# Kernel tuning notes

Hardware: AMD Instinct MI355X
Metric: run time of the kernel (lower is better)

The kernel has to match this reference:

```python
import jax, jax.numpy as jnp
import numpy as np

B, M, L, IN_C, MID_C, OUT_C = 1, 128, 256, 256, 32, 128


def setup_inputs() -> dict:
    key = jax.random.key(0)
    k_x, k_proj, k_final = jax.random.split(key, 3)
    return {
        "x1d": jax.random.normal(k_x, (B, M, L, IN_C), dtype=jnp.float32),
        "norm_w": jnp.ones((IN_C,), dtype=jnp.float32),
        "norm_b": jnp.zeros((IN_C,), dtype=jnp.float32),
        "proj_w": jax.random.normal(k_proj, (2 * MID_C, IN_C), dtype=jnp.float32) * 0.02,
        "proj_b": jnp.zeros((2 * MID_C,), dtype=jnp.float32),
        "final_w": jax.random.normal(k_final, (OUT_C, MID_C * MID_C), dtype=jnp.float32) * 0.02,
        "final_b": jnp.zeros((OUT_C,), dtype=jnp.float32),
    }


def reference(x1d, norm_w, norm_b, proj_w, proj_b, final_w, final_b):
    # LayerNorm over channel dim
    mu = jnp.mean(x1d, axis=-1, keepdims=True)
    var = jnp.mean(jnp.square(x1d - mu), axis=-1, keepdims=True)
    x = (x1d - mu) * jax.lax.rsqrt(var + 1e-5) * norm_w + norm_b

    mid_c = proj_w.shape[0] // 2
    # Linear -> (b, m, L, 2*mid_c); view (..., mid_c, 2); chunk & squeeze:
    # i = interleaved even channels, j = interleaved odd channels
    p = jnp.einsum('bmlc,dc->bmld', x, proj_w) + proj_b
    p = p.reshape(*p.shape[:-1], mid_c, 2)
    i, j = p[..., 0], p[..., 1]          # each (b, m, L, mid_c)

    m = x1d.shape[1]
    # Outer product mean over the MSA (m) dimension -> (b, L, L, mid_c, mid_c)
    x2d = jnp.einsum('bmix,bmjy->bijxy', i, j) / m

    b, li, lj = x2d.shape[0], x2d.shape[1], x2d.shape[2]
    flat = x2d.reshape(b, li, lj, mid_c * mid_c)
    out = jnp.einsum('bijf,of->bijo', flat, final_w) + final_b
    return out
```

## Files before the change

### kernel.cpp

```cpp
#include <hip/hip_runtime.h>

#define DEVINL __device__ __forceinline__

typedef float  f32x4_t  __attribute__((ext_vector_type(4)));
typedef float  f32x16_t __attribute__((ext_vector_type(16)));
typedef short  bf16x8_t __attribute__((ext_vector_type(8)));

#define MFMA16(a,b,c) __builtin_amdgcn_mfma_f32_16x16x32_bf16((a),(b),(c),0,0,0)
#define MFMA32(a,b,c) __builtin_amdgcn_mfma_f32_32x32x16_bf16((a),(b),(c),0,0,0)

DEVINL unsigned short f2bf(float f) {
  union { float f; unsigned u; } v; v.f = f;
  unsigned r = v.u + 0x7fffu + ((v.u >> 16) & 1u);
  return (unsigned short)(r >> 16);
}


__global__ __launch_bounds__(256) void kA(const float* __restrict__ x,
                                          const float* __restrict__ nw,
                                          const float* __restrict__ nb,
                                          const float* __restrict__ pw,
                                          const float* __restrict__ pb,
                                          const float* __restrict__ fw,
                                          unsigned short* __restrict__ Wb,
                                          unsigned short* __restrict__ Ig,
                                          unsigned short* __restrict__ Jg) {
  if (blockIdx.x >= 1024) {
    int i = (blockIdx.x - 1024) * 256 + threadIdx.x;
    float4 v = ((const float4*)fw)[i];
    int o  = i >> 8;
    int f0 = (i & 255) * 4;
    ushort4 u;
    u.x = f2bf(v.x); u.y = f2bf(v.y); u.z = f2bf(v.z); u.w = f2bf(v.w);
    size_t off = (size_t)((o >> 5) * 64 + (f0 >> 4)) * 512 + (o & 31) * 16 + ((f0 >> 3) & 1) * 8 + (f0 & 7);
    *(ushort4*)&Wb[off] = u;
    return;
  }
  __shared__ unsigned short xnl[32 * 264];
  __shared__ unsigned short pwl[64 * 264];
  __shared__ unsigned short ep[64 * 36];
  const int tid  = threadIdx.x;
  const int wv   = tid >> 6;
  const int lane = tid & 63;
  const int q    = lane >> 4;
  const int ln16 = lane & 15;
  const int l    = blockIdx.x & 255;
  const int m0   = (blockIdx.x >> 8) * 32;

  const float4* xs = (const float4*)x;
  float4 v[8];
#pragma unroll
  for (int i = 0; i < 8; i++) {
    int row = m0 + i * 4 + wv;
    v[i] = xs[row * 16384 + l * 64 + lane];
  }
  float4 nw4 = ((const float4*)nw)[lane];
  float4 nb4 = ((const float4*)nb)[lane];

#pragma unroll
  for (int i = 0; i < 8; i++) {
    float s  = v[i].x + v[i].y + v[i].z + v[i].w;
    float ss = v[i].x * v[i].x + v[i].y * v[i].y + v[i].z * v[i].z + v[i].w * v[i].w;
#pragma unroll
    for (int off = 32; off > 0; off >>= 1) {
      s  += __shfl_xor(s, off);
      ss += __shfl_xor(ss, off);
    }
    float mu  = s * (1.0f / 256.0f);
    float var = ss * (1.0f / 256.0f) - mu * mu;
    float rs  = rsqrtf(var + 1e-5f);
    ushort4 u;
    u.x = f2bf((v[i].x - mu) * rs * nw4.x + nb4.x);
    u.y = f2bf((v[i].y - mu) * rs * nw4.y + nb4.y);
    u.z = f2bf((v[i].z - mu) * rs * nw4.z + nb4.z);
    u.w = f2bf((v[i].w - mu) * rs * nw4.w + nb4.w);
    *(ushort4*)&xnl[(i * 4 + wv) * 264 + lane * 4] = u;
  }

  const float4* ps = (const float4*)pw;
#pragma unroll
  for (int i = 0; i < 16; i++) {
    float4 w4 = ps[i * 256 + tid];
    ushort4 u;
    u.x = f2bf(w4.x); u.y = f2bf(w4.y); u.z = f2bf(w4.z); u.w = f2bf(w4.w);
    *(ushort4*)&pwl[(i * 4 + wv) * 264 + lane * 4] = u;
  }
  __syncthreads();

  const int rt = wv & 1;
  const int db = (wv >> 1) * 32;
  f32x4_t acc[2] = {{0.f, 0.f, 0.f, 0.f}, {0.f, 0.f, 0.f, 0.f}};
#pragma unroll
  for (int kc = 0; kc < 8; kc++) {
    bf16x8_t a  = *(const bf16x8_t*)&xnl[(rt * 16 + ln16) * 264 + kc * 32 + q * 8];
    bf16x8_t b0 = *(const bf16x8_t*)&pwl[(db + ln16) * 264 + kc * 32 + q * 8];
    bf16x8_t b1 = *(const bf16x8_t*)&pwl[(db + 16 + ln16) * 264 + kc * 32 + q * 8];
    acc[0] = MFMA16(a, b0, acc[0]);
    acc[1] = MFMA16(a, b1, acc[1]);
  }

#pragma unroll
  for (int t2 = 0; t2 < 2; t2++) {
    int d = db + t2 * 16 + ln16;
    float bias  = pb[d];
    float scale = (d & 1) ? 1.0f : (1.0f / 128.0f);
#pragma unroll
    for (int r = 0; r < 4; r++) {
      int mloc = rt * 16 + q * 4 + r;
      ep[d * 36 + mloc] = f2bf((acc[t2][r] + bias) * scale);
    }
  }
  __syncthreads();

  const int h  = tid >> 3;
  const int m4 = tid & 7;
  const size_t off = (size_t)(l * 8 + (m0 >> 4) + (m4 >> 2)) * 512 + h * 16 + ((m4 >> 1) & 1) * 8 + (m4 & 1) * 4;
  ushort4 vi = *(const ushort4*)&ep[(2 * h) * 36 + m4 * 4];
  *(ushort4*)&Ig[off] = vi;
  ushort4 vj = *(const ushort4*)&ep[(2 * h + 1) * 36 + m4 * 4];
  *(ushort4*)&Jg[off] = vj;
}

__global__ __launch_bounds__(512, 2) void kB(const unsigned short* __restrict__ Ig,
                                             const unsigned short* __restrict__ Jg,
                                             const unsigned short* __restrict__ Wb,
                                             const float* __restrict__ fb,
                                             float* __restrict__ out) {
  extern __shared__ unsigned short fl[];
  const int tid  = threadIdx.x;
  const int w    = tid >> 6;
  const int lane = tid & 63;
  const int ln32 = lane & 31;
  const int h    = lane >> 5;
  const int p    = blockIdx.x >> 3;
  const int t    = blockIdx.x & 7;

  bf16x8_t af[2][8];
#pragma unroll
  for (int il = 0; il < 2; il++)
#pragma unroll
    for (int mc = 0; mc < 8; mc++)
      af[il][mc] = *(const bf16x8_t*)&Ig[(size_t)((p * 2 + il) * 8 + mc) * 512 + ln32 * 16 + h * 8];

  const unsigned short* Jbase = Jg + (size_t)(t * 32 + w * 4) * 4096 + ln32 * 16 + h * 8;
  const int eo = ln32 & 7;
  const int oc = ln32 >> 3;

  bf16x8_t bf[2][8];
#pragma unroll
  for (int mc = 0; mc < 8; mc++) bf[0][mc] = *(const bf16x8_t*)&Jbase[mc * 512];

#pragma unroll
  for (int s = 0; s < 4; s++) {
    if (s < 3) {
#pragma unroll
      for (int mc = 0; mc < 8; mc++)
        bf[(s + 1) & 1][mc] = *(const bf16x8_t*)&Jbase[(s + 1) * 4096 + mc * 512];
    }
    f32x16_t a0, a1;
#pragma unroll
    for (int i = 0; i < 16; i++) { a0[i] = 0.f; a1[i] = 0.f; }
#pragma unroll
    for (int mc = 0; mc < 8; mc++) {
      a0 = MFMA32(af[0][mc], bf[s & 1][mc], a0);
      a1 = MFMA32(af[1][mc], bf[s & 1][mc], a1);
    }
    const int fr = w * 4 + s;
    unsigned short* fr0 = &fl[fr * 1032 + eo];
#pragma unroll
    for (int reg = 0; reg < 16; reg++) {
      int xx  = (reg & 3) + 8 * (reg >> 2) + 4 * h;
      int cp  = ((xx * 4 + oc) ^ (((xx >> 2) & 3) * 5)) * 8;
      fr0[cp]         = f2bf(a0[reg]);
      fr0[33024 + cp] = f2bf(a1[reg]);
    }
  }
  __syncthreads();

  const int il = w >> 2;
  const int ot = w & 3;
  const unsigned short* Wp  = Wb + (size_t)(ot * 64) * 512 + ln32 * 16 + h * 8;
  const unsigned short* flp = fl + il * 33024 + ln32 * 1032;

  f32x16_t oa;
#pragma unroll
  for (int i = 0; i < 16; i++) oa[i] = 0.f;

#define LDA(kc) (*(const bf16x8_t*)&flp[((((kc) >> 1) * 4 + ((kc) & 1) * 2 + h) ^ ((((kc) >> 3) & 3) * 5)) * 8])
  bf16x8_t a0 = LDA(0);
  bf16x8_t b0 = *(const bf16x8_t*)&Wp[0];
  bf16x8_t b1 = *(const bf16x8_t*)&Wp[512];
#pragma unroll 8
  for (int kc = 0; kc < 64; kc++) {
    bf16x8_t an = a0, bn = b1;
    if (kc < 63) an = LDA(kc + 1);
    if (kc < 62) bn = *(const bf16x8_t*)&Wp[(kc + 2) * 512];
    oa = MFMA32(a0, b0, oa);
    a0 = an; b0 = b1; b1 = bn;
  }
#undef LDA

  float bias = fb[ot * 32 + ln32];
  float* op = out + ((size_t)(p * 2 + il) * 256 + t * 32) * 128 + ot * 32 + ln32;
#pragma unroll
  for (int reg = 0; reg < 16; reg++) {
    int row = (reg & 3) + 8 * (reg >> 2) + 4 * h;
    op[row * 128] = oa[reg] + bias;
  }
}

extern "C" void kernel_launch(void* const* d_in, const int* in_sizes, int n_in,
                              void* d_out, int out_size, void* d_ws, size_t ws_size,
                              hipStream_t stream) {
  const float* x1d     = (const float*)d_in[0];
  const float* norm_w  = (const float*)d_in[1];
  const float* norm_b  = (const float*)d_in[2];
  const float* proj_w  = (const float*)d_in[3];
  const float* proj_b  = (const float*)d_in[4];
  const float* final_w = (const float*)d_in[5];
  const float* final_b = (const float*)d_in[6];
  float* outp          = (float*)d_out;

  unsigned short* Wb  = (unsigned short*)d_ws;
  unsigned short* Igp = Wb + 131072;
  unsigned short* Jgp = Igp + 1048576;

  const int kb_lds = 2 * 32 * 1032 * 2;
  hipFuncSetAttribute((const void*)kB, hipFuncAttributeMaxDynamicSharedMemorySize, kb_lds);

  kA<<<1152, 256, 0, stream>>>(x1d, norm_w, norm_b, proj_w, proj_b, final_w, Wb, Igp, Jgp);
  kB<<<1024, 512, kb_lds, stream>>>(Igp, Jgp, Wb, final_b, outp);
}
```

Before: 142.3 us.

## Halve kB tile per block, split K across waves, reduce via LDS

Each kB block now covers 16 j-columns instead of 32, which halves its LDS footprint and doubles the grid. Launch bounds are raised to allow four blocks per CU. The final GEMM is split along K between the two wave groups, and their partial sums are combined through LDS before the output is written. Bf16 conversion now uses a packed two-value intrinsic, and the W fragment loads are prefetched four deep. The trade is an extra LDS reduction and sync, plus tighter register limits at the higher occupancy target.

```diff
diff --git a/kernel.cpp b/kernel.cpp
--- a/kernel.cpp
+++ b/kernel.cpp
@@ -1,4 +1,5 @@
 #include <hip/hip_runtime.h>
+#include <hip/hip_bf16.h>
 
 #define DEVINL __device__ __forceinline__
 
@@ -13,6 +14,12 @@
   union { float f; unsigned u; } v; v.f = f;
   unsigned r = v.u + 0x7fffu + ((v.u >> 16) & 1u);
   return (unsigned short)(r >> 16);
+}
+
+DEVINL unsigned pk2bf(float lo, float hi) {
+  union { __hip_bfloat162 h2; unsigned u; } v;
+  v.h2 = __float22bfloat162_rn(make_float2(lo, hi));
+  return v.u;
 }
 
 
@@ -121,7 +128,7 @@
   *(ushort4*)&Jg[off] = vj;
 }
 
-__global__ __launch_bounds__(512, 2) void kB(const unsigned short* __restrict__ Ig,
+__global__ __launch_bounds__(512, 4) void kB(const unsigned short* __restrict__ Ig,
                                              const unsigned short* __restrict__ Jg,
                                              const unsigned short* __restrict__ Wb,
                                              const float* __restrict__ fb,
@@ -132,8 +139,8 @@
   const int lane = tid & 63;
   const int ln32 = lane & 31;
   const int h    = lane >> 5;
-  const int p    = blockIdx.x >> 3;
-  const int t    = blockIdx.x & 7;
+  const int p    = blockIdx.x >> 4;
+  const int t2   = blockIdx.x & 15;
 
   bf16x8_t af[2][8];
 #pragma unroll
@@ -142,7 +149,7 @@
     for (int mc = 0; mc < 8; mc++)
       af[il][mc] = *(const bf16x8_t*)&Ig[(size_t)((p * 2 + il) * 8 + mc) * 512 + ln32 * 16 + h * 8];
 
-  const unsigned short* Jbase = Jg + (size_t)(t * 32 + w * 4) * 4096 + ln32 * 16 + h * 8;
+  const unsigned short* Jbase = Jg + (size_t)(t2 * 16 + w * 2) * 4096 + ln32 * 16 + h * 8;
   const int eo = ln32 & 7;
   const int oc = ln32 >> 3;
 
@@ -151,61 +158,84 @@
   for (int mc = 0; mc < 8; mc++) bf[0][mc] = *(const bf16x8_t*)&Jbase[mc * 512];
 
 #pragma unroll
-  for (int s = 0; s < 4; s++) {
-    if (s < 3) {
+  for (int s = 0; s < 2; s++) {
+    if (s == 0) {
 #pragma unroll
       for (int mc = 0; mc < 8; mc++)
-        bf[(s + 1) & 1][mc] = *(const bf16x8_t*)&Jbase[(s + 1) * 4096 + mc * 512];
+        bf[1][mc] = *(const bf16x8_t*)&Jbase[4096 + mc * 512];
     }
     f32x16_t a0, a1;
 #pragma unroll
     for (int i = 0; i < 16; i++) { a0[i] = 0.f; a1[i] = 0.f; }
 #pragma unroll
     for (int mc = 0; mc < 8; mc++) {
-      a0 = MFMA32(af[0][mc], bf[s & 1][mc], a0);
-      a1 = MFMA32(af[1][mc], bf[s & 1][mc], a1);
-    }
-    const int fr = w * 4 + s;
+      a0 = MFMA32(af[0][mc], bf[s][mc], a0);
+      a1 = MFMA32(af[1][mc], bf[s][mc], a1);
+    }
+    const int fr = w * 2 + s;
     unsigned short* fr0 = &fl[fr * 1032 + eo];
-#pragma unroll
-    for (int reg = 0; reg < 16; reg++) {
-      int xx  = (reg & 3) + 8 * (reg >> 2) + 4 * h;
-      int cp  = ((xx * 4 + oc) ^ (((xx >> 2) & 3) * 5)) * 8;
-      fr0[cp]         = f2bf(a0[reg]);
-      fr0[33024 + cp] = f2bf(a1[reg]);
-    }
-  }
-  __syncthreads();
-
-  const int il = w >> 2;
+    unsigned short* fr1 = &fl[(16 + fr) * 1032 + eo];
+#pragma unroll
+    for (int rp = 0; rp < 8; rp++) {
+      int x0  = (2 * rp & 3) + 8 * (rp >> 1) + 4 * h;
+      int cp0 = ((x0 * 4 + oc) ^ (((x0 >> 2) & 3) * 5)) * 8;
+      int cp1 = (((x0 + 1) * 4 + oc) ^ ((((x0 + 1) >> 2) & 3) * 5)) * 8;
+      unsigned u0 = pk2bf(a0[2 * rp], a0[2 * rp + 1]);
+      fr0[cp0] = (unsigned short)u0;
+      fr0[cp1] = (unsigned short)(u0 >> 16);
+      unsigned u1 = pk2bf(a1[2 * rp], a1[2 * rp + 1]);
+      fr1[cp0] = (unsigned short)u1;
+      fr1[cp1] = (unsigned short)(u1 >> 16);
+    }
+  }
+
   const int ot = w & 3;
-  const unsigned short* Wp  = Wb + (size_t)(ot * 64) * 512 + ln32 * 16 + h * 8;
-  const unsigned short* flp = fl + il * 33024 + ln32 * 1032;
+  const int kh = w >> 2;
+  const unsigned short* Wp = Wb + (size_t)(ot * 64 + kh * 32) * 512 + ln32 * 16 + h * 8;
+  bf16x8_t bq[4];
+  bq[0] = *(const bf16x8_t*)&Wp[0];
+  bq[1] = *(const bf16x8_t*)&Wp[512];
+
+  __syncthreads();
+
+  bq[2] = *(const bf16x8_t*)&Wp[2 * 512];
+  bq[3] = *(const bf16x8_t*)&Wp[3 * 512];
+
+  const unsigned short* flp = fl + ln32 * 1032;
+#define LDA(kc) (*(const bf16x8_t*)&flp[((((kc) >> 1) * 4 + ((kc) & 1) * 2 + h) ^ ((((kc) >> 3) & 3) * 5)) * 8])
 
   f32x16_t oa;
 #pragma unroll
   for (int i = 0; i < 16; i++) oa[i] = 0.f;
 
-#define LDA(kc) (*(const bf16x8_t*)&flp[((((kc) >> 1) * 4 + ((kc) & 1) * 2 + h) ^ ((((kc) >> 3) & 3) * 5)) * 8])
-  bf16x8_t a0 = LDA(0);
-  bf16x8_t b0 = *(const bf16x8_t*)&Wp[0];
-  bf16x8_t b1 = *(const bf16x8_t*)&Wp[512];
-#pragma unroll 8
-  for (int kc = 0; kc < 64; kc++) {
-    bf16x8_t an = a0, bn = b1;
-    if (kc < 63) an = LDA(kc + 1);
-    if (kc < 62) bn = *(const bf16x8_t*)&Wp[(kc + 2) * 512];
-    oa = MFMA32(a0, b0, oa);
-    a0 = an; b0 = b1; b1 = bn;
+  bf16x8_t a0 = LDA(kh * 32), a1 = LDA(kh * 32 + 1);
+#pragma unroll
+  for (int c = 0; c < 32; c++) {
+    bf16x8_t acur = a0;
+    bf16x8_t bcur = bq[c & 3];
+    if (c < 31) a0 = a1;
+    if (c < 30) a1 = LDA(kh * 32 + c + 2);
+    if (c < 28) bq[c & 3] = *(const bf16x8_t*)&Wp[(c + 4) * 512];
+    oa = MFMA32(acur, bcur, oa);
   }
 #undef LDA
 
-  float bias = fb[ot * 32 + ln32];
-  float* op = out + ((size_t)(p * 2 + il) * 256 + t * 32) * 128 + ot * 32 + ln32;
-#pragma unroll
-  for (int reg = 0; reg < 16; reg++) {
-    int row = (reg & 3) + 8 * (reg >> 2) + 4 * h;
-    op[row * 128] = oa[reg] + bias;
+  __syncthreads();
+  float* red = (float*)fl;
+  if (kh == 1) {
+#pragma unroll
+    for (int r = 0; r < 16; r++) red[(ot * 16 + r) * 64 + lane] = oa[r];
+  }
+  __syncthreads();
+  if (kh == 0) {
+    float bias = fb[ot * 32 + ln32];
+    float* op = out + ((size_t)(p * 2) * 256 + t2 * 16) * 128 + ot * 32 + ln32;
+#pragma unroll
+    for (int r = 0; r < 16; r++) {
+      float val = oa[r] + red[(ot * 16 + r) * 64 + lane] + bias;
+      int row = (r & 3) + 8 * (r >> 2) + 4 * h;
+      op[(row >> 4) * 32768 + (row & 15) * 128] = val;
+    }
   }
 }
 
@@ -225,9 +255,9 @@
   unsigned short* Igp = Wb + 131072;
   unsigned short* Jgp = Igp + 1048576;
 
-  const int kb_lds = 2 * 32 * 1032 * 2;
+  const int kb_lds = 32 * 1032 * 2;
   hipFuncSetAttribute((const void*)kB, hipFuncAttributeMaxDynamicSharedMemorySize, kb_lds);
 
   kA<<<1152, 256, 0, stream>>>(x1d, norm_w, norm_b, proj_w, proj_b, final_w, Wb, Igp, Jgp);
-  kB<<<1024, 512, kb_lds, stream>>>(Igp, Jgp, Wb, final_b, outp);
-}
+  kB<<<2048, 512, kb_lds, stream>>>(Igp, Jgp, Wb, final_b, outp);
+}
```

After: 139.9 us. Within noise of the previous version (-1.7%).
